# Kernel tuning notes

Hardware: AMD Instinct MI355X
Metric: run time of the kernel (lower is better)

## Reference

```python
import jax, jax.numpy as jnp
import numpy as np

N = 8192
F_IN = 128
F_OUT = 128
NEG_SLOPE = 0.2


def setup_inputs() -> dict:
    key = jax.random.key(0)
    k_h, k_adj, k_W, k_a = jax.random.split(key, 4)
    h = jax.random.normal(k_h, (N, F_IN), dtype=jnp.float32)
    # binary adjacency mask as float (the module multiplies scores by adj)
    adj = (jax.random.uniform(k_adj, (N, N)) < 0.05).astype(jnp.float32)
    # nn.Linear(in, out, bias=False): weight shape [out, in]
    W = jax.random.normal(k_W, (F_OUT, F_IN), dtype=jnp.float32) / np.sqrt(F_IN)
    # nn.Linear(2*out, 1, bias=False): weight shape [1, 2*out]
    a = jax.random.normal(k_a, (1, 2 * F_OUT), dtype=jnp.float32) / np.sqrt(2 * F_OUT)
    return {"h": h, "adj": adj, "W": W, "a": a}


def reference(h, adj, W, a):
    # Wh: [N, F_out]
    Wh = h @ W.T
    f = Wh.shape[-1]
    # a([Wh_i ; Wh_j]) factored: e[i, j] = leaky_relu(Wh[i]@a1 + Wh[j]@a2)
    a1 = a[0, :f]  # [F_out]
    a2 = a[0, f:]  # [F_out]
    s_i = Wh @ a1  # [N]
    s_j = Wh @ a2  # [N]
    e = jax.nn.leaky_relu(s_i[:, None] + s_j[None, :], NEG_SLOPE)  # [N, N]
    # faithful to original: softmax over dim=1 of e * adj (multiplicative mask)
    attention = jax.nn.softmax(e * adj, axis=1)  # [N, N]
    return attention @ Wh  # [N, F_out]
```

## Files before the change

### kernel.cpp

```cpp
#include <hip/hip_runtime.h>

#define N_NODES 8192
#define FDIM 128
#define NEG_SLOPE 0.2f
#define CAP 2048

__global__ __launch_bounds__(256) void wh_gemm_kernel(
    const float* __restrict__ h, const float* __restrict__ W,
    float* __restrict__ Wh) {
  __shared__ float Wt[FDIM * 129];
  __shared__ float rows[32 * FDIM];
  const int t = threadIdx.x;
  const int base = blockIdx.x * 32;
  for (int it = 0; it < 64; ++it) {
    int idx = t + 256 * it;
    int o = idx >> 7, k = idx & 127;
    Wt[k * 129 + o] = W[idx];
  }
  for (int it = 0; it < 16; ++it) {
    int idx = t + 256 * it;
    rows[idx] = h[(size_t)base * FDIM + idx];
  }
  __syncthreads();
  const int o = t & 127;
  const int rhalf = t >> 7;
  float acc[16];
#pragma unroll
  for (int kk = 0; kk < 16; ++kk) acc[kk] = 0.f;
  for (int k = 0; k < FDIM; ++k) {
    float wv = Wt[k * 129 + o];
#pragma unroll
    for (int kk = 0; kk < 16; ++kk)
      acc[kk] += rows[(rhalf * 16 + kk) * FDIM + k] * wv;
  }
#pragma unroll
  for (int kk = 0; kk < 16; ++kk) {
    int r = base + rhalf * 16 + kk;
    Wh[(size_t)r * FDIM + o] = acc[kk];
  }
}

__global__ __launch_bounds__(256) void scores_kernel(
    const float* __restrict__ Wh, const float* __restrict__ a,
    float* __restrict__ s1, float* __restrict__ s2) {
  const int t = threadIdx.x;
  const int lane = t & 63;
  const int wave = t >> 6;
  const int row = blockIdx.x * 4 + wave;
  float v0 = Wh[(size_t)row * FDIM + lane];
  float v1 = Wh[(size_t)row * FDIM + 64 + lane];
  float d1 = v0 * a[lane] + v1 * a[64 + lane];
  float d2 = v0 * a[FDIM + lane] + v1 * a[FDIM + 64 + lane];
  for (int off = 32; off; off >>= 1) {
    d1 += __shfl_down(d1, off);
    d2 += __shfl_down(d2, off);
  }
  if (lane == 0) { s1[row] = d1; s2[row] = d2; }
}

__global__ __launch_bounds__(256) void colsum_kernel(
    const float* __restrict__ Wh, float* __restrict__ S) {
  __shared__ float sh[2][FDIM];
  const int t = threadIdx.x;
  const int f = t & 127, seg = t >> 7;
  float acc = 0.f;
  const size_t rbase = (size_t)blockIdx.x * 256 + (size_t)seg * 128;
  for (int k = 0; k < 128; ++k)
    acc += Wh[(rbase + k) * FDIM + f];
  sh[seg][f] = acc;
  __syncthreads();
  if (seg == 0) atomicAdd(&S[f], sh[0][f] + sh[1][f]);
}

__global__ __launch_bounds__(256) void gat_row_kernel(
    const float* __restrict__ adj, const float* __restrict__ Wh,
    const float* __restrict__ s1, const float* __restrict__ s2,
    const float* __restrict__ S, float* __restrict__ out) {
  const int i = blockIdx.x;
  const int t = threadIdx.x;
  const int lane = t & 63;
  const int wave = t >> 6;
  __shared__ int nbr[CAP];
  __shared__ float pv[CAP];
  __shared__ int cnt_s;
  __shared__ float red[4];
  __shared__ float m_sh, l_sh, em_sh;
  __shared__ float fpart[2][FDIM];
  if (t == 0) cnt_s = 0;
  __syncthreads();
  const float s1i = s1[i];
  const float4* __restrict__ arow = (const float4*)(adj + (size_t)i * N_NODES);
  const float4* __restrict__ s2v = (const float4*)s2;
  float lmax = -1e30f;
  for (int it = 0; it < N_NODES / 1024; ++it) {
    const int j4 = it * 256 + t;
    float4 av = arow[j4];
    float4 sv = s2v[j4];
    float avv[4] = {av.x, av.y, av.z, av.w};
    float svv[4] = {sv.x, sv.y, sv.z, sv.w};
    float ecand[4];
    bool pred[4];
#pragma unroll
    for (int c = 0; c < 4; ++c) {
      float e = s1i + svv[c];
      e = e > 0.f ? e : NEG_SLOPE * e;
      ecand[c] = e;
      pred[c] = (avv[c] != 0.f);
      if (pred[c]) lmax = fmaxf(lmax, e);
    }
#pragma unroll
    for (int c = 0; c < 4; ++c) {
      unsigned long long b = __ballot(pred[c]);
      int prefix = __popcll(b & ((1ull << lane) - 1ull));
      int bse = 0;
      if (lane == 0) bse = atomicAdd(&cnt_s, (int)__popcll(b));
      bse = __shfl(bse, 0);
      if (pred[c]) {
        int pos = bse + prefix;
        if (pos < CAP) { nbr[pos] = j4 * 4 + c; pv[pos] = ecand[c]; }
      }
    }
  }
  for (int off = 32; off; off >>= 1) lmax = fmaxf(lmax, __shfl_down(lmax, off));
  if (lane == 0) red[wave] = lmax;
  __syncthreads();
  if (t == 0) {
    float m = fmaxf(fmaxf(red[0], red[1]), fmaxf(red[2], red[3]));
    int cnt = cnt_s;
    if (cnt > CAP) cnt = CAP;
    cnt_s = cnt;
    if (cnt < N_NODES) m = fmaxf(m, 0.f);
    m_sh = m;
  }
  __syncthreads();
  const float m = m_sh;
  const int cnt = cnt_s;
  float lsum = 0.f;
  for (int k = t; k < cnt; k += 256) {
    float p = __expf(pv[k] - m);
    pv[k] = p;
    lsum += p;
  }
  for (int off = 32; off; off >>= 1) lsum += __shfl_down(lsum, off);
  __syncthreads();
  if (lane == 0) red[wave] = lsum;
  __syncthreads();
  if (t == 0) {
    float em = __expf(-m);
    float l = red[0] + red[1] + red[2] + red[3] + (float)(N_NODES - cnt) * em;
    l_sh = l;
    em_sh = em;
  }
  __syncthreads();
  const float l = l_sh, em = em_sh;
  const int f = t & 127, g = t >> 7;
  float a0 = 0.f, a1 = 0.f, a2 = 0.f, a3 = 0.f;
  int k = g;
  for (; k + 6 < cnt; k += 8) {
    a0 += (pv[k]     - em) * Wh[(size_t)nbr[k]     * FDIM + f];
    a1 += (pv[k + 2] - em) * Wh[(size_t)nbr[k + 2] * FDIM + f];
    a2 += (pv[k + 4] - em) * Wh[(size_t)nbr[k + 4] * FDIM + f];
    a3 += (pv[k + 6] - em) * Wh[(size_t)nbr[k + 6] * FDIM + f];
  }
  for (; k < cnt; k += 2)
    a0 += (pv[k] - em) * Wh[(size_t)nbr[k] * FDIM + f];
  fpart[g][f] = a0 + a1 + a2 + a3;
  __syncthreads();
  if (g == 0) {
    float o = (fpart[0][f] + fpart[1][f] + em * S[f]) / l;
    out[(size_t)i * FDIM + f] = o;
  }
}

extern "C" void kernel_launch(void* const* d_in, const int* in_sizes, int n_in,
                              void* d_out, int out_size, void* d_ws, size_t ws_size,
                              hipStream_t stream) {
  const float* h   = (const float*)d_in[0];
  const float* adj = (const float*)d_in[1];
  const float* W   = (const float*)d_in[2];
  const float* a   = (const float*)d_in[3];
  float* out = (float*)d_out;
  float* Wh = (float*)d_ws;
  float* s1 = Wh + (size_t)N_NODES * FDIM;
  float* s2 = s1 + N_NODES;
  float* S  = s2 + N_NODES;

  hipLaunchKernelGGL(wh_gemm_kernel, dim3(N_NODES / 32), dim3(256), 0, stream,
                     h, W, Wh);
  hipLaunchKernelGGL(scores_kernel, dim3(N_NODES / 4), dim3(256), 0, stream,
                     Wh, a, s1, s2);
  hipMemsetAsync(S, 0, FDIM * sizeof(float), stream);
  hipLaunchKernelGGL(colsum_kernel, dim3(32), dim3(256), 0, stream, Wh, S);
  hipLaunchKernelGGL(gat_row_kernel, dim3(N_NODES), dim3(256), 0, stream,
                     adj, Wh, s1, s2, S, out);
}
```

Measured before the change: 477.1 us.

## Use per-wave neighbor lists without atomics and float2 gathers in GAT row kernel

The row kernel now has each wave build its own compacted neighbor list from a running ballot count, replacing the shared atomic counter and the broadcast shuffle. Each wave then accumulates its own neighbors over all 128 features using float2 loads, and the four wave partials are reduced through shared memory. This removes LDS atomics and a barrier and makes each gather a contiguous row read per wave. Other changes pad the GEMM's shared tile rows to 132 and split the column sum over twice as many blocks. The per-wave cap of 512 neighbors per 2048-column segment should hold for 5% density, but any overflow is dropped silently.

```diff
diff --git a/kernel.cpp b/kernel.cpp
--- a/kernel.cpp
+++ b/kernel.cpp
@@ -3,13 +3,13 @@
 #define N_NODES 8192
 #define FDIM 128
 #define NEG_SLOPE 0.2f
-#define CAP 2048
+#define SEG 512
 
 __global__ __launch_bounds__(256) void wh_gemm_kernel(
     const float* __restrict__ h, const float* __restrict__ W,
     float* __restrict__ Wh) {
   __shared__ float Wt[FDIM * 129];
-  __shared__ float rows[32 * FDIM];
+  __shared__ float rows[32 * 132];
   const int t = threadIdx.x;
   const int base = blockIdx.x * 32;
   for (int it = 0; it < 64; ++it) {
@@ -19,7 +19,8 @@
   }
   for (int it = 0; it < 16; ++it) {
     int idx = t + 256 * it;
-    rows[idx] = h[(size_t)base * FDIM + idx];
+    int rloc = idx >> 7, col = idx & 127;
+    rows[rloc * 132 + col] = h[(size_t)base * FDIM + idx];
   }
   __syncthreads();
   const int o = t & 127;
@@ -31,7 +32,7 @@
     float wv = Wt[k * 129 + o];
 #pragma unroll
     for (int kk = 0; kk < 16; ++kk)
-      acc[kk] += rows[(rhalf * 16 + kk) * FDIM + k] * wv;
+      acc[kk] += rows[(rhalf * 16 + kk) * 132 + k] * wv;
   }
 #pragma unroll
   for (int kk = 0; kk < 16; ++kk) {
@@ -64,8 +65,8 @@
   const int t = threadIdx.x;
   const int f = t & 127, seg = t >> 7;
   float acc = 0.f;
-  const size_t rbase = (size_t)blockIdx.x * 256 + (size_t)seg * 128;
-  for (int k = 0; k < 128; ++k)
+  const size_t rbase = (size_t)blockIdx.x * 128 + (size_t)seg * 64;
+  for (int k = 0; k < 64; ++k)
     acc += Wh[(rbase + k) * FDIM + f];
   sh[seg][f] = acc;
   __syncthreads();
@@ -80,17 +81,21 @@
   const int t = threadIdx.x;
   const int lane = t & 63;
   const int wave = t >> 6;
-  __shared__ int nbr[CAP];
-  __shared__ float pv[CAP];
-  __shared__ int cnt_s;
+  __shared__ int nbr[4 * SEG];
+  __shared__ float pv[4 * SEG];
+  __shared__ int counts[4];
   __shared__ float red[4];
   __shared__ float m_sh, l_sh, em_sh;
-  __shared__ float fpart[2][FDIM];
-  if (t == 0) cnt_s = 0;
-  __syncthreads();
+  __shared__ float fpart[4][FDIM];
+
   const float s1i = s1[i];
   const float4* __restrict__ arow = (const float4*)(adj + (size_t)i * N_NODES);
   const float4* __restrict__ s2v = (const float4*)s2;
+  int* __restrict__ mynbr = nbr + wave * SEG;
+  float* __restrict__ mypv = pv + wave * SEG;
+  const unsigned long long lmask = (1ull << lane) - 1ull;
+
+  int base = 0;
   float lmax = -1e30f;
   for (int it = 0; it < N_NODES / 1024; ++it) {
     const int j4 = it * 256 + t;
@@ -111,63 +116,66 @@
 #pragma unroll
     for (int c = 0; c < 4; ++c) {
       unsigned long long b = __ballot(pred[c]);
-      int prefix = __popcll(b & ((1ull << lane) - 1ull));
-      int bse = 0;
-      if (lane == 0) bse = atomicAdd(&cnt_s, (int)__popcll(b));
-      bse = __shfl(bse, 0);
       if (pred[c]) {
-        int pos = bse + prefix;
-        if (pos < CAP) { nbr[pos] = j4 * 4 + c; pv[pos] = ecand[c]; }
+        int pos = base + (int)__popcll(b & lmask);
+        if (pos < SEG) { mynbr[pos] = j4 * 4 + c; mypv[pos] = ecand[c]; }
       }
+      base += (int)__popcll(b);
     }
   }
+  if (lane == 0) counts[wave] = base < SEG ? base : SEG;
   for (int off = 32; off; off >>= 1) lmax = fmaxf(lmax, __shfl_down(lmax, off));
   if (lane == 0) red[wave] = lmax;
   __syncthreads();
   if (t == 0) {
     float m = fmaxf(fmaxf(red[0], red[1]), fmaxf(red[2], red[3]));
-    int cnt = cnt_s;
-    if (cnt > CAP) cnt = CAP;
-    cnt_s = cnt;
+    int cnt = counts[0] + counts[1] + counts[2] + counts[3];
     if (cnt < N_NODES) m = fmaxf(m, 0.f);
     m_sh = m;
   }
   __syncthreads();
   const float m = m_sh;
-  const int cnt = cnt_s;
+  const int mycnt = counts[wave];
   float lsum = 0.f;
-  for (int k = t; k < cnt; k += 256) {
-    float p = __expf(pv[k] - m);
-    pv[k] = p;
+  for (int k = lane; k < mycnt; k += 64) {
+    float p = __expf(mypv[k] - m);
+    mypv[k] = p;
     lsum += p;
   }
   for (int off = 32; off; off >>= 1) lsum += __shfl_down(lsum, off);
-  __syncthreads();
   if (lane == 0) red[wave] = lsum;
   __syncthreads();
   if (t == 0) {
+    int cnt = counts[0] + counts[1] + counts[2] + counts[3];
     float em = __expf(-m);
-    float l = red[0] + red[1] + red[2] + red[3] + (float)(N_NODES - cnt) * em;
-    l_sh = l;
+    l_sh = red[0] + red[1] + red[2] + red[3] + (float)(N_NODES - cnt) * em;
     em_sh = em;
   }
   __syncthreads();
   const float l = l_sh, em = em_sh;
-  const int f = t & 127, g = t >> 7;
-  float a0 = 0.f, a1 = 0.f, a2 = 0.f, a3 = 0.f;
-  int k = g;
-  for (; k + 6 < cnt; k += 8) {
-    a0 += (pv[k]     - em) * Wh[(size_t)nbr[k]     * FDIM + f];
-    a1 += (pv[k + 2] - em) * Wh[(size_t)nbr[k + 2] * FDIM + f];
-    a2 += (pv[k + 4] - em) * Wh[(size_t)nbr[k + 4] * FDIM + f];
-    a3 += (pv[k + 6] - em) * Wh[(size_t)nbr[k + 6] * FDIM + f];
-  }
-  for (; k < cnt; k += 2)
-    a0 += (pv[k] - em) * Wh[(size_t)nbr[k] * FDIM + f];
-  fpart[g][f] = a0 + a1 + a2 + a3;
-  __syncthreads();
-  if (g == 0) {
-    float o = (fpart[0][f] + fpart[1][f] + em * S[f]) / l;
+  const float2* __restrict__ Wh2 = (const float2*)Wh;
+  float a0x = 0.f, a0y = 0.f, a1x = 0.f, a1y = 0.f;
+  int k = 0;
+  for (; k + 1 < mycnt; k += 2) {
+    float w0 = mypv[k] - em, w1 = mypv[k + 1] - em;
+    int j0 = mynbr[k], j1 = mynbr[k + 1];
+    float2 v0 = Wh2[(size_t)j0 * 64 + lane];
+    float2 v1 = Wh2[(size_t)j1 * 64 + lane];
+    a0x += w0 * v0.x; a0y += w0 * v0.y;
+    a1x += w1 * v1.x; a1y += w1 * v1.y;
+  }
+  if (k < mycnt) {
+    float w0 = mypv[k] - em;
+    float2 v0 = Wh2[(size_t)mynbr[k] * 64 + lane];
+    a0x += w0 * v0.x; a0y += w0 * v0.y;
+  }
+  fpart[wave][2 * lane]     = a0x + a1x;
+  fpart[wave][2 * lane + 1] = a0y + a1y;
+  __syncthreads();
+  if (t < FDIM) {
+    int f = t;
+    float o = (fpart[0][f] + fpart[1][f] + fpart[2][f] + fpart[3][f]
+               + em * S[f]) / l;
     out[(size_t)i * FDIM + f] = o;
   }
 }
@@ -190,7 +198,7 @@
   hipLaunchKernelGGL(scores_kernel, dim3(N_NODES / 4), dim3(256), 0, stream,
                      Wh, a, s1, s2);
   hipMemsetAsync(S, 0, FDIM * sizeof(float), stream);
-  hipLaunchKernelGGL(colsum_kernel, dim3(32), dim3(256), 0, stream, Wh, S);
+  hipLaunchKernelGGL(colsum_kernel, dim3(64), dim3(256), 0, stream, Wh, S);
   hipLaunchKernelGGL(gat_row_kernel, dim3(N_NODES), dim3(256), 0, stream,
                      adj, Wh, s1, s2, S, out);
 }
```

Result: no change. 467.8 us (-1.9%).
